# Kernel tuning notes

Hardware: AMD Instinct MI355X
Metric: run time of the kernel (lower is better)

The kernel has to match this reference:

```python
import jax, jax.numpy as jnp
import numpy as np

G = 8          # n_games
D_IN = 512     # per-game input dim (equal for all games)
H1 = 1024
H2 = 1024
A = 128        # max_actions
B = 8192       # batch rows


def setup_inputs() -> dict:
    key = jax.random.key(0)
    ks = jax.random.split(key, 9)
    state = jax.random.normal(ks[0], (B, D_IN), dtype=jnp.float32)
    idx = jax.random.randint(ks[1], (B,), 0, G, dtype=jnp.int32)
    # per-game input linears: uniform(-1/sqrt(fan_in), 1/sqrt(fan_in))
    lim1 = 1.0 / np.sqrt(D_IN)
    W1 = jax.random.uniform(ks[2], (G, D_IN, H1), minval=-lim1, maxval=lim1, dtype=jnp.float32)
    b1 = jax.random.uniform(ks[3], (G, H1), minval=-lim1, maxval=lim1, dtype=jnp.float32)
    # shared linear
    lim2 = 1.0 / np.sqrt(H1)
    W2 = jax.random.uniform(ks[4], (H1, H2), minval=-lim2, maxval=lim2, dtype=jnp.float32)
    b2 = jax.random.uniform(ks[5], (H2,), minval=-lim2, maxval=lim2, dtype=jnp.float32)
    # per-game output heads: uniform(-0.003, 0.003)
    W3 = jax.random.uniform(ks[6], (G, H2, A), minval=-0.003, maxval=0.003, dtype=jnp.float32)
    b3 = jax.random.uniform(ks[7], (G, A), minval=-0.003, maxval=0.003, dtype=jnp.float32)
    return {"state": state, "idx": idx, "W1": W1, "b1": b1, "W2": W2, "b2": b2, "W3": W3, "b3": b3}


def reference(state, idx, W1, b1, W2, b2, W3, b3):
    # Torch code concatenates per-game groups in sorted-unique-idx order,
    # i.e. a stable permutation of rows by idx; reproduce exactly.
    perm = jnp.argsort(idx, stable=True)          # [B]
    s = state[perm]                               # [B, D_IN]
    g = idx[perm]                                 # [B] game of each permuted row
    # routed first layer: compute all games then gather per-row game
    h1_all = jnp.einsum('bd,gdh->bgh', s, W1) + b1            # [B, G, H1]
    h1 = jax.nn.relu(jnp.take_along_axis(h1_all, g[:, None, None], axis=1)[:, 0, :])  # [B, H1]
    h_f = jax.nn.relu(h1 @ W2 + b2)                            # [B, H2]
    a = jnp.tanh(jnp.einsum('bh,gha->bga', h_f, W3) + b3)      # [B, G, A]
    # NOTE: original gathers heads with the ORIGINAL (unpermuted) idx,
    # even though rows of `a` are in permuted order. Reproduce faithfully.
    out = jnp.take_along_axis(a, idx[:, None, None], axis=1)[:, 0, :]  # [B, A]
    return out
```

## Files before the change

kernel.cpp:

```cpp
#include <hip/hip_runtime.h>
#include <math.h>

#define G_GAMES 8
#define D_IN 512
#define H1 1024
#define H2 1024
#define A_DIM 128
#define B_ROWS 8192

typedef short bf16x8 __attribute__((ext_vector_type(8)));
typedef float f32x4 __attribute__((ext_vector_type(4)));

#define WS_OFF   0u
#define WS_PERM  256u
#define WS_SPERM 33280u
#define WS_W1T   (WS_SPERM + B_ROWS*D_IN*2u)
#define WS_W2T   (WS_W1T + G_GAMES*D_IN*H1*2u)
#define WS_W3T   (WS_W2T + (unsigned)H1*H2*2u)
#define WS_H1    (WS_W3T + G_GAMES*H2*A_DIM*2u)
#define WS_HF    WS_SPERM

__device__ __forceinline__ unsigned short f2bf(float x) {
  union { float f; unsigned int u; } v; v.f = x;
  unsigned int r = v.u + 0x7fffu + ((v.u >> 16) & 1u);
  return (unsigned short)(r >> 16);
}

__device__ __forceinline__ void async_load16(const void* gptr, void* ldsptr) {
  __builtin_amdgcn_global_load_lds(
      (const __attribute__((address_space(1))) unsigned int*)gptr,
      (__attribute__((address_space(3))) unsigned int*)ldsptr,
      16, 0, 0);
}

__device__ void sort_256(const int* __restrict__ idx, int* __restrict__ perm,
                         int* __restrict__ off) {
  __shared__ int wtot[4][9];
  __shared__ int wbase[4][9];
  __shared__ int offs[9];
  const int t = threadIdx.x, lane = t & 63, wave = t >> 6;
  int my[32];
#pragma unroll
  for (int i = 0; i < 8; ++i) {
    const int4 a = *(const int4*)(idx + t * 32 + i * 4);
    my[i*4+0] = a.x; my[i*4+1] = a.y; my[i*4+2] = a.z; my[i*4+3] = a.w;
  }
  int local[8] = {0,0,0,0,0,0,0,0};
#pragma unroll
  for (int i = 0; i < 32; ++i) local[my[i]]++;
  int incl[8];
#pragma unroll
  for (int g = 0; g < 8; ++g) {
    int v = local[g];
#pragma unroll
    for (int d = 1; d < 64; d <<= 1) {
      const int n = __shfl_up(v, d);
      if (lane >= d) v += n;
    }
    incl[g] = v;
  }
  if (lane == 63) {
#pragma unroll
    for (int g = 0; g < 8; ++g) wtot[wave][g] = incl[g];
  }
  __syncthreads();
  if (t < 8) {
    int s = 0;
#pragma unroll
    for (int w = 0; w < 4; ++w) { wbase[w][t] = s; s += wtot[w][t]; }
    wtot[0][t] = s;
  }
  __syncthreads();
  if (t == 0) {
    int s = 0;
#pragma unroll
    for (int g = 0; g < 8; ++g) { offs[g] = s; off[g] = s; s += wtot[0][g]; }
    offs[8] = s; off[8] = s;
  }
  __syncthreads();
  int start[8];
#pragma unroll
  for (int g = 0; g < 8; ++g)
    start[g] = offs[g] + wbase[wave][g] + (incl[g] - local[g]);
#pragma unroll
  for (int i = 0; i < 32; ++i) {
    const int g = my[i];
    perm[start[g]++] = t * 32 + i;
  }
}

__device__ void trans_tile(const float* __restrict__ in,
                           unsigned short* __restrict__ out,
                           int R, int C, int xt, int yt, int z) {
  in  += (size_t)z * R * C;
  out += (size_t)z * R * C;
  __shared__ float tile[64][65];
  const int c0 = xt * 64, r0 = yt * 64;
  const int tx = threadIdx.x & 63, ty = threadIdx.x >> 6;
#pragma unroll
  for (int rr = ty; rr < 64; rr += 4)
    tile[rr][tx] = in[(size_t)(r0 + rr) * C + c0 + tx];
  __syncthreads();
#pragma unroll
  for (int cc = ty; cc < 64; cc += 4)
    out[(size_t)(c0 + cc) * R + r0 + tx] = f2bf(tile[tx][cc]);
}

__global__ __launch_bounds__(256) void k_pre1(const float* __restrict__ W1,
                                              const float* __restrict__ W2,
                                              const float* __restrict__ W3,
                                              const int* __restrict__ idx,
                                              unsigned short* __restrict__ W1T,
                                              unsigned short* __restrict__ W2T,
                                              unsigned short* __restrict__ W3T,
                                              int* __restrict__ perm,
                                              int* __restrict__ off) {
  const int b = blockIdx.x;
  if (b < 1024) {
    const int z = b >> 7, r = b & 127;
    trans_tile(W1, W1T, D_IN, H1, r & 15, r >> 4, z);
  } else if (b < 1280) {
    const int r = b - 1024;
    trans_tile(W2, W2T, H1, H2, r & 15, r >> 4, 0);
  } else if (b < 1536) {
    const int r = (b - 1280) & 31, z = (b - 1280) >> 5;
    trans_tile(W3, W3T, H2, A_DIM, r & 1, r >> 1, z);
  } else {
    sort_256(idx, perm, off);
  }
}

__global__ __launch_bounds__(256) void k_gather(const float* __restrict__ state,
                                                const int* __restrict__ perm,
                                                unsigned short* __restrict__ sPerm) {
  const int p = blockIdx.x * 2 + (threadIdx.x >> 7);
  const int c = (threadIdx.x & 127) << 2;
  const int src = perm[p];
  const float4 v = *(const float4*)(state + (size_t)src * D_IN + c);
  ushort4 o;
  o.x = f2bf(v.x); o.y = f2bf(v.y); o.z = f2bf(v.z); o.w = f2bf(v.w);
  *(ushort4*)(sPerm + (size_t)p * D_IN + c) = o;
}

template <int KTOT>
__device__ __forceinline__ void gemm_db64(const unsigned short* const* aP,
                                          const unsigned short* const* bP,
                                          char* smem, int tid, f32x4 acc[4][2]) {
  const int lane = tid & 63, wave = tid >> 6;
  const int wm = wave & 1, wn = wave >> 1;
  const int sw = lane & 15, quad = lane >> 4;
  const int mA = wm * 64 + sw;
  const int nB = wn * 32 + sw;
  char* A0 = smem;          char* A1 = smem + 16384;
  char* B0 = smem + 32768;  char* B1 = smem + 40960;
  const int NIT = KTOT >> 6;
#pragma unroll
  for (int c = 0; c < 4; ++c)
    async_load16(aP[c], A0 + (wave * 32 + c * 8) * 128);
#pragma unroll
  for (int c = 0; c < 2; ++c)
    async_load16(bP[c], B0 + (wave * 16 + c * 8) * 128);
#pragma unroll 2
  for (int k = 0; k < NIT; ++k) {
    __syncthreads();
    char* A = (k & 1) ? A1 : A0;
    char* B = (k & 1) ? B1 : B0;
    if (k + 1 < NIT) {
      char* An = (k & 1) ? A0 : A1;
      char* Bn = (k & 1) ? B0 : B1;
      const int koff = (k + 1) << 6;
#pragma unroll
      for (int c = 0; c < 4; ++c)
        async_load16(aP[c] + koff, An + (wave * 32 + c * 8) * 128);
#pragma unroll
      for (int c = 0; c < 2; ++c)
        async_load16(bP[c] + koff, Bn + (wave * 16 + c * 8) * 128);
    }
#pragma unroll
    for (int ks = 0; ks < 2; ++ks) {
      const int u = ((((ks << 2) + quad) ^ (sw & 7)) << 4);
      bf16x8 aF[4], bF[2];
#pragma unroll
      for (int i = 0; i < 4; ++i)
        aF[i] = *(const bf16x8*)(A + (mA + i * 16) * 128 + u);
#pragma unroll
      for (int j = 0; j < 2; ++j)
        bF[j] = *(const bf16x8*)(B + (nB + j * 16) * 128 + u);
#pragma unroll
      for (int i = 0; i < 4; ++i)
#pragma unroll
        for (int j = 0; j < 2; ++j)
          acc[i][j] = __builtin_amdgcn_mfma_f32_16x16x32_bf16(aF[i], bF[j], acc[i][j], 0, 0, 0);
    }
  }
}

__device__ __forceinline__ bool seg_map(const int* __restrict__ off, int T,
                                        int& g, int& seg1, int& row0) {
  int base = 0;
  for (int gg = 0; gg < 8; ++gg) {
    const int s = off[gg], e = off[gg + 1];
    const int nt = (e - s + 127) >> 7;
    if (T < base + nt) { g = gg; seg1 = e; row0 = s + (T - base) * 128; return true; }
    base += nt;
  }
  return false;
}

__device__ __forceinline__ bool seg_map32(const int* __restrict__ off, int T,
                                          int& g, int& seg1, int& row0) {
  int base = 0;
  for (int gg = 0; gg < 8; ++gg) {
    const int s = off[gg], e = off[gg + 1];
    const int nt = (e - s + 31) >> 5;
    if (T < base + nt) { g = gg; seg1 = e; row0 = s + (T - base) * 32; return true; }
    base += nt;
  }
  return false;
}

__device__ __forceinline__ void epilogue64(char* smem, const f32x4 acc[4][2],
                                           const float* bj, int tid,
                                           unsigned short* __restrict__ outp,
                                           size_t ldOut, int row0, int col0,
                                           int vrows) {
  const int lane = tid & 63, wave = tid >> 6;
  const int wm = wave & 1, wn = wave >> 1;
  const int sw = lane & 15, quad = lane >> 4;
  __syncthreads();
#pragma unroll
  for (int i = 0; i < 4; ++i)
#pragma unroll
    for (int j = 0; j < 2; ++j)
#pragma unroll
      for (int r = 0; r < 4; ++r) {
        const int row = wm * 64 + i * 16 + quad * 4 + r;
        const int col = wn * 32 + j * 16 + sw;
        const float v = fmaxf(acc[i][j][r] + bj[j], 0.0f);
        *(unsigned short*)(smem + row * 136 + col * 2) = f2bf(v);
      }
  __syncthreads();
#pragma unroll
  for (int q = 0; q < 4; ++q) {
    const int idxq = q * 256 + tid;
    const int row = idxq >> 3, ch = idxq & 7;
    if (row < vrows) {
      const uint2 lo = *(const uint2*)(smem + row * 136 + ch * 16);
      const uint2 hi = *(const uint2*)(smem + row * 136 + ch * 16 + 8);
      uint4 v; v.x = lo.x; v.y = lo.y; v.z = hi.x; v.w = hi.y;
      *(uint4*)((char*)outp + ((size_t)(row0 + row) * ldOut + col0 + ch * 8) * 2) = v;
    }
  }
}

__global__ __launch_bounds__(256) void k_gemm1(const unsigned short* __restrict__ sPerm,
                                               const unsigned short* __restrict__ W1T,
                                               const float* __restrict__ b1,
                                               const int* __restrict__ off,
                                               unsigned short* __restrict__ h1out) {
  __shared__ char smem[49152];
  int g, seg1, row0;
  if (!seg_map(off, blockIdx.x, g, seg1, row0)) return;
  const int col0 = blockIdx.y * 64;
  const int tid = threadIdx.x, lane = tid & 63, wave = tid >> 6;
  const int gcol = ((lane & 7) ^ (lane >> 3)) << 3;
  const unsigned short* aP[4];
  const unsigned short* bP[2];
#pragma unroll
  for (int c = 0; c < 4; ++c) {
    const int rl = wave * 32 + c * 8 + (lane >> 3);
    int p = row0 + rl;
    if (p > seg1 - 1) p = seg1 - 1;
    aP[c] = sPerm + (size_t)p * D_IN + gcol;
  }
#pragma unroll
  for (int c = 0; c < 2; ++c) {
    const int rl = wave * 16 + c * 8 + (lane >> 3);
    bP[c] = W1T + (size_t)g * H1 * D_IN + (size_t)(col0 + rl) * D_IN + gcol;
  }
  f32x4 acc[4][2] = {};
  gemm_db64<D_IN>(aP, bP, smem, tid, acc);
  const int wn = wave >> 1, sw = lane & 15;
  const float* bg = b1 + g * H1;
  float bj[2];
#pragma unroll
  for (int j = 0; j < 2; ++j) bj[j] = bg[col0 + wn * 32 + j * 16 + sw];
  const int vrows = min(128, seg1 - row0);
  epilogue64(smem, acc, bj, tid, h1out, H1, row0, col0, vrows);
}

__global__ __launch_bounds__(256) void k_gemm2(const unsigned short* __restrict__ h1in,
                                               const unsigned short* __restrict__ W2T,
                                               const float* __restrict__ b2,
                                               unsigned short* __restrict__ hfout) {
  __shared__ char smem[49152];
  const int bid = blockIdx.x;
  const int xcd = bid & 7, s = bid >> 3;
  const int row0 = (xcd * 8 + (s & 7)) * 128;
  const int col0 = (s >> 3) * 64;
  const int tid = threadIdx.x, lane = tid & 63, wave = tid >> 6;
  const int gcol = ((lane & 7) ^ (lane >> 3)) << 3;
  const unsigned short* aP[4];
  const unsigned short* bP[2];
#pragma unroll
  for (int c = 0; c < 4; ++c) {
    const int rl = wave * 32 + c * 8 + (lane >> 3);
    aP[c] = h1in + (size_t)(row0 + rl) * H1 + gcol;
  }
#pragma unroll
  for (int c = 0; c < 2; ++c) {
    const int rl = wave * 16 + c * 8 + (lane >> 3);
    bP[c] = W2T + (size_t)(col0 + rl) * H1 + gcol;
  }
  f32x4 acc[4][2] = {};
  gemm_db64<H1>(aP, bP, smem, tid, acc);
  const int wn = wave >> 1, sw = lane & 15;
  float bj[2];
#pragma unroll
  for (int j = 0; j < 2; ++j) bj[j] = b2[col0 + wn * 32 + j * 16 + sw];
  epilogue64(smem, acc, bj, tid, hfout, H2, row0, col0, 128);
}

__global__ __launch_bounds__(256) void k_gemm3(const unsigned short* __restrict__ hf,
                                               const unsigned short* __restrict__ W3T,
                                               const float* __restrict__ b3,
                                               const int* __restrict__ off,
                                               const int* __restrict__ perm,
                                               float* __restrict__ outp) {
  __shared__ char smem[40960];
  int g, seg1, row0;
  if (!seg_map32(off, blockIdx.x, g, seg1, row0)) return;
  const int tid = threadIdx.x, lane = tid & 63, wave = tid >> 6;
  const int wm = wave & 1, wn = wave >> 1;
  const int sw = lane & 15, quad = lane >> 4;
  const int gcol = ((lane & 7) ^ (lane >> 3)) << 3;
  int q0 = row0 + wave * 8 + (lane >> 3);
  if (q0 > seg1 - 1) q0 = seg1 - 1;
  const unsigned short* aP = hf + (size_t)perm[q0] * H2 + gcol;
  const unsigned short* bP[4];
#pragma unroll
  for (int c = 0; c < 4; ++c) {
    const int rl = wave * 32 + c * 8 + (lane >> 3);
    bP[c] = W3T + (size_t)g * A_DIM * H2 + (size_t)rl * H2 + gcol;
  }
  char* A0 = smem;         char* A1 = smem + 4096;
  char* B0 = smem + 8192;  char* B1 = smem + 24576;
  const int mA = wm * 16 + sw;
  const int nB = wn * 64 + sw;
  f32x4 acc[4] = {};
  async_load16(aP, A0 + (wave * 8) * 128);
#pragma unroll
  for (int c = 0; c < 4; ++c)
    async_load16(bP[c], B0 + (wave * 32 + c * 8) * 128);
#pragma unroll 2
  for (int k = 0; k < (H2 >> 6); ++k) {
    __syncthreads();
    char* A = (k & 1) ? A1 : A0;
    char* B = (k & 1) ? B1 : B0;
    if (k + 1 < (H2 >> 6)) {
      char* An = (k & 1) ? A0 : A1;
      char* Bn = (k & 1) ? B0 : B1;
      const int koff = (k + 1) << 6;
      async_load16(aP + koff, An + (wave * 8) * 128);
#pragma unroll
      for (int c = 0; c < 4; ++c)
        async_load16(bP[c] + koff, Bn + (wave * 32 + c * 8) * 128);
    }
#pragma unroll
    for (int ks = 0; ks < 2; ++ks) {
      const int u = ((((ks << 2) + quad) ^ (sw & 7)) << 4);
      const bf16x8 aF = *(const bf16x8*)(A + mA * 128 + u);
      bf16x8 bF[4];
#pragma unroll
      for (int j = 0; j < 4; ++j)
        bF[j] = *(const bf16x8*)(B + (nB + j * 16) * 128 + u);
#pragma unroll
      for (int j = 0; j < 4; ++j)
        acc[j] = __builtin_amdgcn_mfma_f32_16x16x32_bf16(aF, bF[j], acc[j], 0, 0, 0);
    }
  }
  const float* bg = b3 + g * A_DIM;
  float bj[4];
#pragma unroll
  for (int j = 0; j < 4; ++j) bj[j] = bg[wn * 64 + j * 16 + sw];
  __syncthreads();
#pragma unroll
  for (int j = 0; j < 4; ++j)
#pragma unroll
    for (int r = 0; r < 4; ++r) {
      const int row = wm * 16 + quad * 4 + r;
      const int col = wn * 64 + j * 16 + sw;
      *(float*)(smem + row * 528 + col * 4) = tanhf(acc[j][r] + bj[j]);
    }
  __syncthreads();
#pragma unroll
  for (int qq = 0; qq < 4; ++qq) {
    const int idxq = qq * 256 + tid;
    const int row = idxq >> 5, ch = idxq & 31;
    if (row0 + row < seg1) {
      const uint4 v = *(const uint4*)(smem + row * 528 + ch * 16);
      *(uint4*)((char*)outp + ((size_t)perm[row0 + row] * A_DIM + ch * 4) * 4) = v;
    }
  }
}

extern "C" void kernel_launch(void* const* d_in, const int* in_sizes, int n_in,
                              void* d_out, int out_size, void* d_ws, size_t ws_size,
                              hipStream_t stream) {
  (void)in_sizes; (void)n_in; (void)out_size; (void)ws_size;
  const float* state = (const float*)d_in[0];
  const int*   idx   = (const int*)d_in[1];
  const float* W1    = (const float*)d_in[2];
  const float* b1    = (const float*)d_in[3];
  const float* W2    = (const float*)d_in[4];
  const float* b2    = (const float*)d_in[5];
  const float* W3    = (const float*)d_in[6];
  const float* b3    = (const float*)d_in[7];
  float* outp = (float*)d_out;
  char* ws = (char*)d_ws;
  int* off  = (int*)(ws + WS_OFF);
  int* perm = (int*)(ws + WS_PERM);
  unsigned short* sPerm = (unsigned short*)(ws + WS_SPERM);
  unsigned short* W1T   = (unsigned short*)(ws + WS_W1T);
  unsigned short* W2T   = (unsigned short*)(ws + WS_W2T);
  unsigned short* W3T   = (unsigned short*)(ws + WS_W3T);
  unsigned short* h1    = (unsigned short*)(ws + WS_H1);
  unsigned short* hf    = (unsigned short*)(ws + WS_HF);

  hipLaunchKernelGGL(k_pre1, dim3(1537), dim3(256), 0, stream,
                     W1, W2, W3, idx, W1T, W2T, W3T, perm, off);
  hipLaunchKernelGGL(k_gather, dim3(B_ROWS / 2), dim3(256), 0, stream, state, perm, sPerm);
  hipLaunchKernelGGL(k_gemm1, dim3(72, 16), dim3(256), 0, stream, sPerm, W1T, b1, off, h1);
  hipLaunchKernelGGL(k_gemm2, dim3(1024), dim3(256), 0, stream, h1, W2T, b2, hf);
  hipLaunchKernelGGL(k_gemm3, dim3(264), dim3(256), 0, stream, hf, W3T, b3, off, perm, outp);
}
```

Baseline: 156.7 us.

## Triple-buffer GEMM K-loop with LDS atomic flag sync instead of barriers

Replaces the double-buffered K-loop in gemm1 and gemm2 with a three-slot pipeline that keeps up to three tiles of async global-to-LDS loads in flight. Each stage is gated by an explicit vmcnt wait. Block-wide __syncthreads is replaced by per-stage arrive/done counters in LDS that waves increment atomically and spin on, so waves can drift apart instead of hitting a full barrier every iteration. The aim is to hide load latency and barrier stalls. In exchange, LDS use per block rises from 48KB to 72KB, which can lower occupancy, and the busy-wait spin loops add LDS traffic and some risk to correctness.

```diff
diff --git a/kernel.cpp b/kernel.cpp
--- a/kernel.cpp
+++ b/kernel.cpp
@@ -142,55 +142,76 @@
   *(ushort4*)(sPerm + (size_t)p * D_IN + c) = o;
 }
 
-template <int KTOT>
-__device__ __forceinline__ void gemm_db64(const unsigned short* const* aP,
+#define SLOT_SZ 24576
+
+template <int NIT>
+__device__ __forceinline__ void gemm_pipe(const unsigned short* const* aP,
                                           const unsigned short* const* bP,
-                                          char* smem, int tid, f32x4 acc[4][2]) {
+                                          char* smem, int* flags,
+                                          int tid, f32x4 acc[4][2]) {
   const int lane = tid & 63, wave = tid >> 6;
   const int wm = wave & 1, wn = wave >> 1;
   const int sw = lane & 15, quad = lane >> 4;
   const int mA = wm * 64 + sw;
   const int nB = wn * 32 + sw;
-  char* A0 = smem;          char* A1 = smem + 16384;
-  char* B0 = smem + 32768;  char* B1 = smem + 40960;
-  const int NIT = KTOT >> 6;
-#pragma unroll
-  for (int c = 0; c < 4; ++c)
-    async_load16(aP[c], A0 + (wave * 32 + c * 8) * 128);
-#pragma unroll
-  for (int c = 0; c < 2; ++c)
-    async_load16(bP[c], B0 + (wave * 16 + c * 8) * 128);
-#pragma unroll 2
+  int* arrive = flags;
+  int* done = flags + NIT;
+  volatile int* varr = arrive;
+  volatile int* vdone = done;
+  if (tid < NIT) { arrive[tid] = 0; done[tid] = 0; }
+  __syncthreads();
+#pragma unroll
+  for (int t = 0; t < 3; ++t) {
+    char* As = smem + t * SLOT_SZ;
+    char* Bs = As + 16384;
+    const int koff = t << 6;
+#pragma unroll
+    for (int c = 0; c < 4; ++c)
+      async_load16(aP[c] + koff, As + (wave * 32 + c * 8) * 128);
+#pragma unroll
+    for (int c = 0; c < 2; ++c)
+      async_load16(bP[c] + koff, Bs + (wave * 16 + c * 8) * 128);
+  }
+#pragma unroll
   for (int k = 0; k < NIT; ++k) {
-    __syncthreads();
-    char* A = (k & 1) ? A1 : A0;
-    char* B = (k & 1) ? B1 : B0;
-    if (k + 1 < NIT) {
-      char* An = (k & 1) ? A0 : A1;
-      char* Bn = (k & 1) ? B0 : B1;
-      const int koff = (k + 1) << 6;
-#pragma unroll
-      for (int c = 0; c < 4; ++c)
-        async_load16(aP[c] + koff, An + (wave * 32 + c * 8) * 128);
-#pragma unroll
-      for (int c = 0; c < 2; ++c)
-        async_load16(bP[c] + koff, Bn + (wave * 16 + c * 8) * 128);
-    }
+    if (k <= NIT - 3)      asm volatile("s_waitcnt vmcnt(12)" ::: "memory");
+    else if (k == NIT - 2) asm volatile("s_waitcnt vmcnt(6)" ::: "memory");
+    else                   asm volatile("s_waitcnt vmcnt(0)" ::: "memory");
+    if (lane == 0) atomicAdd(&arrive[k], 1);
+    while (varr[k] < 4) { }
+    asm volatile("" ::: "memory");
+    char* As = smem + (k % 3) * SLOT_SZ;
+    char* Bs = As + 16384;
 #pragma unroll
     for (int ks = 0; ks < 2; ++ks) {
       const int u = ((((ks << 2) + quad) ^ (sw & 7)) << 4);
       bf16x8 aF[4], bF[2];
 #pragma unroll
       for (int i = 0; i < 4; ++i)
-        aF[i] = *(const bf16x8*)(A + (mA + i * 16) * 128 + u);
+        aF[i] = *(const bf16x8*)(As + (mA + i * 16) * 128 + u);
 #pragma unroll
       for (int j = 0; j < 2; ++j)
-        bF[j] = *(const bf16x8*)(B + (nB + j * 16) * 128 + u);
+        bF[j] = *(const bf16x8*)(Bs + (nB + j * 16) * 128 + u);
 #pragma unroll
       for (int i = 0; i < 4; ++i)
 #pragma unroll
         for (int j = 0; j < 2; ++j)
           acc[i][j] = __builtin_amdgcn_mfma_f32_16x16x32_bf16(aF[i], bF[j], acc[i][j], 0, 0, 0);
+    }
+    asm volatile("" ::: "memory");
+    if (lane == 0) atomicAdd(&done[k], 1);
+    if (k + 3 < NIT) {
+      while (vdone[k] < 4) { }
+      asm volatile("" ::: "memory");
+      char* As2 = smem + ((k + 3) % 3) * SLOT_SZ;
+      char* Bs2 = As2 + 16384;
+      const int koff = (k + 3) << 6;
+#pragma unroll
+      for (int c = 0; c < 4; ++c)
+        async_load16(aP[c] + koff, As2 + (wave * 32 + c * 8) * 128);
+#pragma unroll
+      for (int c = 0; c < 2; ++c)
+        async_load16(bP[c] + koff, Bs2 + (wave * 16 + c * 8) * 128);
     }
   }
 }
@@ -258,7 +279,8 @@
                                                const float* __restrict__ b1,
                                                const int* __restrict__ off,
                                                unsigned short* __restrict__ h1out) {
-  __shared__ char smem[49152];
+  __shared__ char smem[3 * SLOT_SZ];
+  __shared__ int flags[16];
   int g, seg1, row0;
   if (!seg_map(off, blockIdx.x, g, seg1, row0)) return;
   const int col0 = blockIdx.y * 64;
@@ -279,7 +301,7 @@
     bP[c] = W1T + (size_t)g * H1 * D_IN + (size_t)(col0 + rl) * D_IN + gcol;
   }
   f32x4 acc[4][2] = {};
-  gemm_db64<D_IN>(aP, bP, smem, tid, acc);
+  gemm_pipe<D_IN / 64>(aP, bP, smem, flags, tid, acc);
   const int wn = wave >> 1, sw = lane & 15;
   const float* bg = b1 + g * H1;
   float bj[2];
@@ -293,7 +315,8 @@
                                                const unsigned short* __restrict__ W2T,
                                                const float* __restrict__ b2,
                                                unsigned short* __restrict__ hfout) {
-  __shared__ char smem[49152];
+  __shared__ char smem[3 * SLOT_SZ];
+  __shared__ int flags[32];
   const int bid = blockIdx.x;
   const int xcd = bid & 7, s = bid >> 3;
   const int row0 = (xcd * 8 + (s & 7)) * 128;
@@ -313,7 +336,7 @@
     bP[c] = W2T + (size_t)(col0 + rl) * H1 + gcol;
   }
   f32x4 acc[4][2] = {};
-  gemm_db64<H1>(aP, bP, smem, tid, acc);
+  gemm_pipe<H1 / 64>(aP, bP, smem, flags, tid, acc);
   const int wn = wave >> 1, sw = lane & 15;
   float bj[2];
 #pragma unroll
```

After: 177.2 us. 1.13x slower.
